# Kernel tuning notes

Measured on AMD Instinct MI355X. Metric: run time of the kernel, lower is better.

Reference implementation:

```python
import jax, jax.numpy as jnp
import numpy as np

B, T, C, H, HD = 2, 2048, 2048, 16, 128
RD = HD // 2          # rope_dim = 64 (32 complex pairs)
KVR, QR = 512, 1024   # kv_lora_rank, q_lora_rank


def setup_inputs() -> dict:
    key = jax.random.key(0)
    ks = jax.random.split(key, 10)
    s = 0.02
    x = jax.random.normal(ks[0], (B, T, C), jnp.float32)
    w_dq  = jax.random.normal(ks[1], (C, QR),     jnp.float32) * s
    w_uq  = jax.random.normal(ks[2], (QR, H * HD), jnp.float32) * s
    w_dkv = jax.random.normal(ks[3], (C, KVR),    jnp.float32) * s
    w_uk  = jax.random.normal(ks[4], (KVR, H * HD), jnp.float32) * s
    w_uv  = jax.random.normal(ks[5], (KVR, H * HD), jnp.float32) * s
    w_qr  = jax.random.normal(ks[6], (QR, H * RD), jnp.float32) * s
    w_kr  = jax.random.normal(ks[7], (C, H * RD), jnp.float32) * s
    w_o   = jax.random.normal(ks[8], (H * HD, C), jnp.float32) * s
    # rotary frequencies for the rope_dim part (rope_dim//2 = 32 complex freqs)
    inv_freq = 1.0 / (10000.0 ** (jnp.arange(0, RD, 2, dtype=jnp.float32) / RD))
    ang = jnp.arange(T, dtype=jnp.float32)[:, None] * inv_freq[None, :]  # (T, 32)
    return {"x": x, "w_dq": w_dq, "w_uq": w_uq, "w_dkv": w_dkv, "w_uk": w_uk,
            "w_uv": w_uv, "w_qr": w_qr, "w_kr": w_kr, "w_o": w_o,
            "freqs_cos": jnp.cos(ang), "freqs_sin": jnp.sin(ang)}


def _apply_rope(t, cos, sin):
    # t: (B, T, H, rd); cos/sin: (T, rd//2). Complex rotation on adjacent pairs.
    tr, ti = t[..., 0::2], t[..., 1::2]
    c = cos[None, :, None, :]
    s = sin[None, :, None, :]
    out_r = tr * c - ti * s
    out_i = tr * s + ti * c
    return jnp.stack([out_r, out_i], axis=-1).reshape(t.shape)


def reference(x, w_dq, w_uq, w_dkv, w_uk, w_uv, w_qr, w_kr, w_o, freqs_cos, freqs_sin):
    b, t, _ = x.shape
    # low-rank KV path
    c_kv = x @ w_dkv                                   # (B,T,KVR)
    k_c = (c_kv @ w_uk).reshape(b, t, H, HD)
    v   = (c_kv @ w_uv).reshape(b, t, H, HD)
    # low-rank Q path
    c_q = x @ w_dq                                     # (B,T,QR)
    q_c = (c_q @ w_uq).reshape(b, t, H, HD)
    # decoupled rope parts
    q_r = (c_q @ w_qr).reshape(b, t, H, RD)
    k_r = (x @ w_kr).reshape(b, t, H, RD)
    q_r = _apply_rope(q_r, freqs_cos, freqs_sin)
    k_r = _apply_rope(k_r, freqs_cos, freqs_sin)
    # concat content + rope -> head dim D = HD + RD
    q = jnp.concatenate([q_c, q_r], axis=-1).transpose(0, 2, 1, 3)  # (B,H,T,D)
    k = jnp.concatenate([k_c, k_r], axis=-1).transpose(0, 2, 1, 3)
    v = v.transpose(0, 2, 1, 3)                                     # (B,H,T,HD)
    d = q.shape[-1]
    scores = jnp.einsum('bhqd,bhkd->bhqk', q, k) / jnp.sqrt(jnp.float32(d))
    causal = jnp.tril(jnp.ones((t, t), dtype=bool))
    scores = jnp.where(causal[None, None], scores, jnp.float32(-1e30))
    att = jax.nn.softmax(scores, axis=-1)
    out = jnp.einsum('bhqk,bhkd->bhqd', att, v)        # (B,H,T,HD)
    out = out.transpose(0, 2, 1, 3).reshape(b, t, H * HD)
    return out @ w_o
```

## Files before the change

kernel.cpp:

```cpp
#include <hip/hip_runtime.h>

typedef unsigned short ushort_t;
typedef __attribute__((ext_vector_type(8))) short bs8;
typedef __attribute__((ext_vector_type(4))) float f32x4;
typedef __attribute__((ext_vector_type(4))) unsigned short u16x4;

#define DEV __device__ __forceinline__

DEV unsigned short f2bf(float f){
  unsigned u = __float_as_uint(f);
  u += 0x7fffu + ((u >> 16) & 1u);
  return (unsigned short)(u >> 16);
}
DEV float bf2f(unsigned short h){ return __uint_as_float(((unsigned)h) << 16); }

DEV unsigned cvt_pk_bf16(float lo, float hi){
  unsigned r;
  asm volatile("v_cvt_pk_bf16_f32 %0, %1, %2" : "=v"(r) : "v"(lo), "v"(hi));
  return r;
}

DEV void gl2lds16(const void* g, void* l){
  __builtin_amdgcn_global_load_lds((const __attribute__((address_space(1))) void*)g,
                                   (__attribute__((address_space(3))) void*)l, 16, 0, 0);
}

DEV void st_out(ushort_t* C, size_t i, float v){ C[i] = f2bf(v); }
DEV void st_out(float*    C, size_t i, float v){ C[i] = v; }

__global__ __launch_bounds__(256) void cast_x(const float* __restrict__ in,
                                              ushort_t* __restrict__ outb){
  size_t i = ((size_t)blockIdx.x * 256 + threadIdx.x) * 4;
  float4 v = *(const float4*)(in + i);
  u16x4 o;
  o[0] = f2bf(v.x); o[1] = f2bf(v.y); o[2] = f2bf(v.z); o[3] = f2bf(v.w);
  *(u16x4*)(outb + i) = o;
}

__global__ __launch_bounds__(256) void tcast_all(
    const float* __restrict__ s0, const float* __restrict__ s1,
    const float* __restrict__ s2, const float* __restrict__ s3,
    const float* __restrict__ s4, const float* __restrict__ s5,
    const float* __restrict__ s6, const float* __restrict__ s7,
    ushort_t* __restrict__ d0, ushort_t* __restrict__ d1,
    ushort_t* __restrict__ d2, ushort_t* __restrict__ d3,
    ushort_t* __restrict__ d4, ushort_t* __restrict__ d5,
    ushort_t* __restrict__ d6, ushort_t* __restrict__ d7){
  __shared__ float tile[32][33];
  const int bid = blockIdx.x;
  const float* src; ushort_t* dst; int K, N, loc;
  if      (bid <  2048){ src=s0; dst=d0; K=2048; N=1024; loc=bid; }
  else if (bid <  3072){ src=s1; dst=d1; K=2048; N=512;  loc=bid-2048; }
  else if (bid <  5120){ src=s2; dst=d2; K=2048; N=1024; loc=bid-3072; }
  else if (bid <  7168){ src=s3; dst=d3; K=1024; N=2048; loc=bid-5120; }
  else if (bid <  8192){ src=s4; dst=d4; K=1024; N=1024; loc=bid-7168; }
  else if (bid <  9216){ src=s5; dst=d5; K=512;  N=2048; loc=bid-8192; }
  else if (bid < 10240){ src=s6; dst=d6; K=512;  N=2048; loc=bid-9216; }
  else                 { src=s7; dst=d7; K=2048; N=2048; loc=bid-10240; }
  const int nx = N >> 5;
  const int n0 = (loc % nx) << 5, k0 = (loc / nx) << 5;
  const int tx = threadIdx.x & 31, ty = threadIdx.x >> 5;
  for (int r = ty; r < 32; r += 8)
    tile[r][tx] = src[(size_t)(k0 + r) * N + n0 + tx];
  __syncthreads();
  for (int r = ty; r < 32; r += 8)
    dst[(size_t)(n0 + r) * K + k0 + tx] = f2bf(tile[tx][r]);
}

__global__ __launch_bounds__(256) void transpose_v(const ushort_t* __restrict__ v, int ldv,
                                                   ushort_t* __restrict__ vT){
  __shared__ ushort_t tile[32][33];
  int bh = blockIdx.z; int b = bh >> 4, h = bh & 15;
  int t0 = blockIdx.x * 32, d0 = blockIdx.y * 32;
  int tx = threadIdx.x, ty = threadIdx.y;
  for (int r = ty; r < 32; r += 8)
    tile[r][tx] = v[((size_t)(b * 2048 + t0 + r)) * ldv + h * 128 + d0 + tx];
  __syncthreads();
  for (int r = ty; r < 32; r += 8)
    vT[((size_t)bh * 128 + d0 + r) * 2048 + t0 + tx] = tile[tx][r];
}

DEV void gemm_core(const ushort_t* __restrict__ A, int lda,
                   const ushort_t* __restrict__ BT, int K,
                   int m0, int n0, ushort_t* lds, f32x4 (&acc)[8][4]){
  const int tid = threadIdx.x, lane = tid & 63, wid = tid >> 6;
  const int l15 = lane & 15, lhi = lane >> 4;
  const int wr = wid >> 2, wc = wid & 3;

  const int trow = tid >> 3;
  const int tcsrc = (tid & 7) ^ (trow & 7);
  const ushort_t* gA[2][2];
  const ushort_t* gB[2][2];
#pragma unroll
  for (int h = 0; h < 2; ++h)
#pragma unroll
    for (int i = 0; i < 2; ++i){
      gA[h][i] = A  + (size_t)(m0 + h * 128 + i * 64 + trow) * lda + tcsrc * 8;
      gB[h][i] = BT + (size_t)(n0 + h * 128 + i * 64 + trow) * K   + tcsrc * 8;
    }

  auto STAGE_A = [&](int buf, int h, int kt){
    gl2lds16(gA[h][0] + (size_t)kt * 64, lds + buf * 32768 + h * 8192 + tid * 8);
    gl2lds16(gA[h][1] + (size_t)kt * 64, lds + buf * 32768 + h * 8192 + 4096 + tid * 8);
  };
  auto STAGE_B = [&](int buf, int h, int kt){
    gl2lds16(gB[h][0] + (size_t)kt * 64, lds + buf * 32768 + 16384 + h * 8192 + tid * 8);
    gl2lds16(gB[h][1] + (size_t)kt * 64, lds + buf * 32768 + 16384 + h * 8192 + 4096 + tid * 8);
  };

  const int ck0 = ((lhi) ^ (l15 & 7)) << 3;
  const int ck1 = ((4 + lhi) ^ (l15 & 7)) << 3;

  bs8 aF[4][2], bLo[2][2], bHi[2][2];

  auto RDA = [&](int buf, int mq){
#pragma unroll
    for (int m = 0; m < 4; ++m){
      const ushort_t* r = lds + buf * 32768 + wr * 8192 + ((mq + m) * 16 + l15) * 64;
      aF[m][0] = *(const bs8*)(r + ck0);
      aF[m][1] = *(const bs8*)(r + ck1);
    }
  };
  auto RDB = [&](int buf, int nq, bs8 (&br)[2][2]){
#pragma unroll
    for (int n = 0; n < 2; ++n){
      const ushort_t* r = lds + buf * 32768 + 16384 + (wc >> 1) * 8192 +
                          ((wc & 1) * 64 + (nq + n) * 16 + l15) * 64;
      br[n][0] = *(const bs8*)(r + ck0);
      br[n][1] = *(const bs8*)(r + ck1);
    }
  };
  auto MMA = [&](int mq, int nq, bs8 (&br)[2][2]){
    __builtin_amdgcn_s_setprio(1);
#pragma unroll
    for (int m = 0; m < 4; ++m)
#pragma unroll
      for (int n = 0; n < 2; ++n){
        acc[mq + m][nq + n] = __builtin_amdgcn_mfma_f32_16x16x32_bf16(aF[m][0], br[n][0], acc[mq + m][nq + n], 0, 0, 0);
        acc[mq + m][nq + n] = __builtin_amdgcn_mfma_f32_16x16x32_bf16(aF[m][1], br[n][1], acc[mq + m][nq + n], 0, 0, 0);
      }
    __builtin_amdgcn_s_setprio(0);
  };

#define BAR() __builtin_amdgcn_s_barrier()
#define LGK() asm volatile("s_waitcnt lgkmcnt(0)" ::: "memory")
#define VMC4() asm volatile("s_waitcnt vmcnt(4)" ::: "memory")

  const int nkt = K >> 6;
  const int nIter = K >> 7;

  STAGE_A(0, 0, 0); STAGE_A(0, 1, 0); STAGE_B(0, 0, 0); STAGE_B(0, 1, 0);
  STAGE_B(1, 0, 1); STAGE_B(1, 1, 1);
  VMC4();
  BAR();

  for (int it = 0; it < nIter; ++it){
    const int kt1 = 2 * it + 1;
    int kt2 = 2 * it + 2; if (kt2 > nkt - 1) kt2 = nkt - 1;
    int kt3 = 2 * it + 3; if (kt3 > nkt - 1) kt3 = nkt - 1;
    RDA(0, 0); RDB(0, 0, bLo);
    STAGE_A(1, 0, kt1);
    BAR(); LGK(); MMA(0, 0, bLo); BAR();
    RDB(0, 2, bHi);
    STAGE_A(1, 1, kt1);
    BAR(); LGK(); MMA(0, 2, bHi); BAR();
    RDA(0, 4);
    STAGE_B(0, 0, kt2);
    BAR(); LGK(); MMA(4, 0, bLo); BAR();
    STAGE_B(0, 1, kt2);
    BAR(); LGK(); MMA(4, 2, bHi);
    VMC4(); BAR();
    RDA(1, 0); RDB(1, 0, bLo);
    STAGE_A(0, 0, kt2);
    BAR(); LGK(); MMA(0, 0, bLo); BAR();
    RDB(1, 2, bHi);
    STAGE_A(0, 1, kt2);
    BAR(); LGK(); MMA(0, 2, bHi); BAR();
    RDA(1, 4);
    STAGE_B(1, 0, kt3);
    BAR(); LGK(); MMA(4, 0, bLo); BAR();
    STAGE_B(1, 1, kt3);
    BAR(); LGK(); MMA(4, 2, bHi);
    VMC4(); BAR();
  }
#undef BAR
#undef LGK
#undef VMC4
}

template<int EPI, typename OT>
DEV void gemm_epi(f32x4 (&acc)[8][4], OT* __restrict__ C, int N, int m0, int n0,
                  ushort_t* __restrict__ aux,
                  const float* __restrict__ fcp, const float* __restrict__ fsp){
  const int tid = threadIdx.x, lane = tid & 63, wid = tid >> 6;
  const int l15 = lane & 15, lhi = lane >> 4;
  const int wr = wid >> 2, wc = wid & 3;
  const float SC = (EPI == 2) ? (0.07216878364870323f * 1.4426950408889634f) : 1.0f;
  const int RBASE = (EPI == 1) ? 1536 : 2048;
#pragma unroll
  for (int m = 0; m < 8; ++m){
    const int r = m0 + wr * 128 + m * 16 + lhi * 4;
#pragma unroll
    for (int n = 0; n < 4; ++n){
      const int c = n0 + wc * 64 + n * 16 + l15;
      if (EPI == 0){
#pragma unroll
        for (int j = 0; j < 4; ++j)
          st_out(C, (size_t)(r + j) * N + c, acc[m][n][j]);
      } else if ((EPI == 1 && c < 1536)){
#pragma unroll
        for (int j = 0; j < 4; ++j)
          C[(size_t)(r + j) * 1536 + c] = (OT)f2bf(acc[m][n][j]);
      } else if (EPI == 2 && c < 2048){
        int hh = c >> 7, d = c & 127;
#pragma unroll
        for (int j = 0; j < 4; ++j){
          int rr = r + j, bb = rr >> 11, tt = rr & 2047;
          aux[((size_t)(bb * 16 + hh) * 2048 + tt) * 192 + d] = f2bf(acc[m][n][j] * SC);
        }
      } else if (EPI == 3 && c < 2048){
        int hh = c >> 7, d = c & 127;
#pragma unroll
        for (int j = 0; j < 4; ++j){
          int rr = r + j, bb = rr >> 11, tt = rr & 2047;
          aux[((size_t)(bb * 16 + hh) * 2048 + tt) * 192 + d] = f2bf(acc[m][n][j]);
        }
      } else if (EPI == 3){
#pragma unroll
        for (int j = 0; j < 4; ++j)
          C[(size_t)(r + j) * 2048 + (c - 2048)] = (OT)f2bf(acc[m][n][j]);
      } else {
        int cr = c - RBASE;
        int hh = cr >> 6, dr = cr & 63, ii = dr >> 1;
#pragma unroll
        for (int j = 0; j < 4; ++j){
          int rr = r + j, bb = rr >> 11, tt = rr & 2047;
          float v = acc[m][n][j] * SC;
          float pv = __shfl_xor(v, 1);
          float co = fcp[tt * 32 + ii], si = fsp[tt * 32 + ii];
          float o = (l15 & 1) ? fmaf(pv, si, v * co) : fmaf(-pv, si, v * co);
          aux[((size_t)(bb * 16 + hh) * 2048 + tt) * 192 + 128 + dr] = f2bf(o);
        }
      }
    }
  }
}

template<int EPI, typename OT>
__global__ __launch_bounds__(512, 2) void gemm256(const ushort_t* __restrict__ A, int lda,
                                                  const ushort_t* __restrict__ BT,
                                                  OT* __restrict__ C,
                                                  int M, int N, int K,
                                                  ushort_t* __restrict__ aux,
                                                  const float* __restrict__ fcp,
                                                  const float* __restrict__ fsp){
  __shared__ __align__(16) ushort_t lds[65536];
  const int nbx = M >> 8;
  const int nwg = gridDim.x;
  const int orig = blockIdx.x;
  const int wg = (orig & 7) * (nwg >> 3) + (orig >> 3);
  const int m0 = (wg % nbx) << 8;
  const int n0 = (wg / nbx) << 8;
  f32x4 acc[8][4] = {};
  gemm_core(A, lda, BT, K, m0, n0, lds, acc);
  gemm_epi<EPI, OT>(acc, C, N, m0, n0, aux, fcp, fsp);
}

__global__ __launch_bounds__(512, 2) void gemm23(const ushort_t* __restrict__ A2,
                                                 const ushort_t* __restrict__ BT2,
                                                 const ushort_t* __restrict__ A3,
                                                 const ushort_t* __restrict__ BT3,
                                                 ushort_t* __restrict__ vb,
                                                 ushort_t* __restrict__ Qa,
                                                 ushort_t* __restrict__ Ka,
                                                 const float* __restrict__ fcp,
                                                 const float* __restrict__ fsp){
  __shared__ __align__(16) ushort_t lds[65536];
  const int nwg = gridDim.x;
  const int orig = blockIdx.x;
  const int wg = (orig & 7) * (nwg >> 3) + (orig >> 3);
  f32x4 acc[8][4] = {};
  if (wg < 192){
    const int m0 = (wg % 16) << 8, n0 = (wg / 16) << 8;
    gemm_core(A2, 1536, BT2, 1024, m0, n0, lds, acc);
    gemm_epi<2, ushort_t>(acc, nullptr, 3072, m0, n0, Qa, fcp, fsp);
  } else {
    const int g = wg - 192;
    const int m0 = (g % 16) << 8, n0 = (g / 16) << 8;
    gemm_core(A3, 1536, BT3, 512, m0, n0, lds, acc);
    gemm_epi<3, ushort_t>(acc, vb, 4096, m0, n0, Ka, fcp, fsp);
  }
}

__global__ __launch_bounds__(512, 1) void gemm4_128(const ushort_t* __restrict__ A, int lda,
                                                    const ushort_t* __restrict__ BT,
                                                    float* __restrict__ C,
                                                    int M, int N, int K){
  __shared__ __align__(16) ushort_t lds[49152];
  const int tid = threadIdx.x, lane = tid & 63, wid = tid >> 6;
  const int l15 = lane & 15, lhi = lane >> 4;
  const int wr = wid >> 1, wc = wid & 1;

  const int nbx = M >> 8;
  const int nwg = gridDim.x;
  const int orig = blockIdx.x;
  const int wg = (orig & 7) * (nwg >> 3) + (orig >> 3);
  const int m0 = (wg % nbx) << 8;
  const int n0 = (wg / nbx) << 7;

  const int trow = tid >> 3;
  const int tcsrc = (tid & 7) ^ (trow & 7);
  const ushort_t* gA[2][2];
  const ushort_t* gB[2];
#pragma unroll
  for (int h = 0; h < 2; ++h)
#pragma unroll
    for (int i = 0; i < 2; ++i)
      gA[h][i] = A + (size_t)(m0 + h * 128 + i * 64 + trow) * lda + tcsrc * 8;
#pragma unroll
  for (int i = 0; i < 2; ++i)
    gB[i] = BT + (size_t)(n0 + i * 64 + trow) * K + tcsrc * 8;

  auto STAGE_A = [&](int buf, int h, int kt){
    gl2lds16(gA[h][0] + (size_t)kt * 64, lds + buf * 24576 + h * 8192 + tid * 8);
    gl2lds16(gA[h][1] + (size_t)kt * 64, lds + buf * 24576 + h * 8192 + 4096 + tid * 8);
  };
  auto STAGE_B = [&](int buf, int kt){
    gl2lds16(gB[0] + (size_t)kt * 64, lds + buf * 24576 + 16384 + tid * 8);
    gl2lds16(gB[1] + (size_t)kt * 64, lds + buf * 24576 + 16384 + 4096 + tid * 8);
  };

  const int ck0 = ((lhi) ^ (l15 & 7)) << 3;
  const int ck1 = ((4 + lhi) ^ (l15 & 7)) << 3;

  f32x4 acc[4][4] = {};
  bs8 aF[2][2], bLo[2][2], bHi[2][2];

  auto RDA = [&](int buf, int mq){
#pragma unroll
    for (int m = 0; m < 2; ++m){
      const int rowin = (wr & 1) * 64 + (mq + m) * 16 + l15;
      const ushort_t* r = lds + buf * 24576 + (wr >> 1) * 8192 + rowin * 64;
      aF[m][0] = *(const bs8*)(r + ck0);
      aF[m][1] = *(const bs8*)(r + ck1);
    }
  };
  auto RDB = [&](int buf, int nq, bs8 (&br)[2][2]){
#pragma unroll
    for (int n = 0; n < 2; ++n){
      const int row = wc * 64 + (nq + n) * 16 + l15;
      const ushort_t* r = lds + buf * 24576 + 16384 + row * 64;
      br[n][0] = *(const bs8*)(r + ck0);
      br[n][1] = *(const bs8*)(r + ck1);
    }
  };
  auto MMA = [&](int mq, int nq, bs8 (&br)[2][2]){
    __builtin_amdgcn_s_setprio(1);
#pragma unroll
    for (int m = 0; m < 2; ++m)
#pragma unroll
      for (int n = 0; n < 2; ++n){
        acc[mq + m][nq + n] = __builtin_amdgcn_mfma_f32_16x16x32_bf16(aF[m][0], br[n][0], acc[mq + m][nq + n], 0, 0, 0);
        acc[mq + m][nq + n] = __builtin_amdgcn_mfma_f32_16x16x32_bf16(aF[m][1], br[n][1], acc[mq + m][nq + n], 0, 0, 0);
      }
    __builtin_amdgcn_s_setprio(0);
  };

#define BAR() __builtin_amdgcn_s_barrier()
#define LGK() asm volatile("s_waitcnt lgkmcnt(0)" ::: "memory")
#define VMC2() asm volatile("s_waitcnt vmcnt(2)" ::: "memory")

  const int nkt = K >> 6;
  const int nIter = K >> 7;

  STAGE_A(0, 0, 0); STAGE_A(0, 1, 0); STAGE_B(0, 0);
  STAGE_B(1, 1);
  VMC2();
  BAR();

  for (int it = 0; it < nIter; ++it){
    const int kt1 = 2 * it + 1;
    int kt2 = 2 * it + 2; if (kt2 > nkt - 1) kt2 = nkt - 1;
    int kt3 = 2 * it + 3; if (kt3 > nkt - 1) kt3 = nkt - 1;
    RDA(0, 0); RDB(0, 0, bLo);
    STAGE_A(1, 0, kt1);
    BAR(); LGK(); MMA(0, 0, bLo); BAR();
    RDB(0, 2, bHi);
    STAGE_A(1, 1, kt1);
    BAR(); LGK(); MMA(0, 2, bHi); BAR();
    RDA(0, 2);
    STAGE_B(0, kt2);
    BAR(); LGK(); MMA(2, 0, bLo); BAR();
    BAR(); LGK(); MMA(2, 2, bHi);
    VMC2(); BAR();
    RDA(1, 0); RDB(1, 0, bLo);
    STAGE_A(0, 0, kt2);
    BAR(); LGK(); MMA(0, 0, bLo); BAR();
    RDB(1, 2, bHi);
    STAGE_A(0, 1, kt2);
    BAR(); LGK(); MMA(0, 2, bHi); BAR();
    RDA(1, 2);
    STAGE_B(1, kt3);
    BAR(); LGK(); MMA(2, 0, bLo); BAR();
    BAR(); LGK(); MMA(2, 2, bHi);
    VMC2(); BAR();
  }
#undef BAR
#undef LGK
#undef VMC2

#pragma unroll
  for (int m = 0; m < 4; ++m){
    const int r = m0 + wr * 64 + m * 16 + lhi * 4;
#pragma unroll
    for (int n = 0; n < 4; ++n){
      const int c = n0 + wc * 64 + n * 16 + l15;
#pragma unroll
      for (int j = 0; j < 4; ++j)
        C[(size_t)(r + j) * N + c] = acc[m][n][j];
    }
  }
}

__global__ __launch_bounds__(512, 1) void attn_kernel(const ushort_t* __restrict__ Qa,
                                                      const ushort_t* __restrict__ Ka,
                                                      const ushort_t* __restrict__ VT,
                                                      ushort_t* __restrict__ O){
  __shared__ __align__(16) ushort_t lds[40960];
  const int tid = threadIdx.x, lane = tid & 63, wid = tid >> 6;
  const int bh = blockIdx.x, p = blockIdx.y;
  const int b = bh >> 4, h = bh & 15;
  const int qb0 = 15 - p, qb1 = p;
  const int nkt0 = 2 * qb0 + 2;
  const int NT = 34;
  const int l15 = lane & 15, lhi = lane >> 4;

  const ushort_t* Kbh = Ka + (size_t)bh * 2048 * 192;
  const ushort_t* Vbh = VT + (size_t)bh * 128 * 2048;

  const ushort_t* ksrc[3];
#pragma unroll
  for (int i = 0; i < 3; ++i){
    int c = i * 512 + tid;
    int row = c / 24, col = c % 24;
    int hk = (row & 3) | (((row >> 3) & 1) << 2);
    ksrc[i] = Kbh + (size_t)row * 192 + (col ^ hk) * 8;
  }
  const ushort_t* vsrc[2];
#pragma unroll
  for (int i = 0; i < 2; ++i){
    int c = i * 512 + tid;
    int d = c >> 3, col = c & 7;
    vsrc[i] = Vbh + (size_t)d * 2048 + (col ^ (d & 7)) * 8;
  }

  auto STAGE = [&](int ft, int buf){
    int kt = (ft < nkt0) ? ft : ft - nkt0;
#pragma unroll
    for (int i = 0; i < 3; ++i)
      gl2lds16(ksrc[i] + (size_t)kt * 12288, lds + buf * 12288 + (i * 512 + tid) * 8);
#pragma unroll
    for (int i = 0; i < 2; ++i)
      gl2lds16(vsrc[i] + kt * 64, lds + 24576 + buf * 8192 + (i * 512 + tid) * 8);
  };

  bs8 qf[6];
  auto LOADQ = [&](int qb){
    const size_t qrow = ((size_t)bh * 2048 + qb * 128 + wid * 16 + l15) * 192;
#pragma unroll
    for (int kc = 0; kc < 6; ++kc)
      qf[kc] = *(const bs8*)(Qa + qrow + kc * 32 + lhi * 8);
  };

  f32x4 acc[8] = {};
  float mrow = -1e30f, lrow = 0.f;

  auto EPI = [&](int qb){
    float rl = 1.0f / lrow;
    int t = qb * 128 + wid * 16 + l15;
#pragma unroll
    for (int f = 0; f < 8; ++f){
      u16x4 o;
#pragma unroll
      for (int j = 0; j < 4; ++j) o[j] = f2bf(acc[f][j] * rl);
      *(u16x4*)(O + ((size_t)b * 2048 + t) * 2048 + h * 128 + f * 16 + lhi * 4) = o;
    }
  };

  const int hkr = (l15 & 3) | (((l15 >> 2) & 1) << 2);

#define BARR() __builtin_amdgcn_s_barrier()
#define LGK0() asm volatile("s_waitcnt lgkmcnt(0)" ::: "memory")
#define VMC(n) asm volatile("s_waitcnt vmcnt(" #n ")" ::: "memory")

  LOADQ(qb0);
  STAGE(0, 0);
  STAGE(1, 1);
  VMC(5);
  BARR();

  for (int ft = 0; ft < NT; ++ft){
    if (ft == nkt0){
      EPI(qb0);
#pragma unroll
      for (int f = 0; f < 8; ++f) acc[f] = (f32x4){0.f, 0.f, 0.f, 0.f};
      mrow = -1e30f; lrow = 0.f;
      LOADQ(qb1);
    }
    const int seg = (ft >= nkt0) ? 1 : 0;
    const int kt = seg ? ft - nkt0 : ft;
    const int qb = seg ? qb1 : qb0;
    const int qm0 = qb << 7;
    const int mylast = 2 * qb + (wid >> 2);
    const int cur = ft & 1;
    const ushort_t* Kb = lds + cur * 12288;
    const ushort_t* Vb = lds + 24576 + cur * 8192;

    if (kt <= mylast){
      f32x4 s[4] = {};
      __builtin_amdgcn_s_setprio(1);
#pragma unroll
      for (int kc = 0; kc < 6; ++kc){
        bs8 kf4[4];
#pragma unroll
        for (int m = 0; m < 4; ++m){
          int row = ((m >> 1) << 5) + ((l15 >> 2) << 3) + ((m & 1) << 2) + (l15 & 3);
          kf4[m] = *(const bs8*)(Kb + row * 192 + (((kc * 4 + lhi) ^ hkr) << 3));
        }
#pragma unroll
        for (int m = 0; m < 4; ++m)
          s[m] = __builtin_amdgcn_mfma_f32_16x16x32_bf16(kf4[m], qf[kc], s[m], 0, 0, 0);
      }
      __builtin_amdgcn_s_setprio(0);

      const bool noMask = (kt * 64 + 63) <= (qm0 + wid * 16);
      const int qi = qm0 + wid * 16 + l15;
      float rmax = -3e38f;
#pragma unroll
      for (int m = 0; m < 4; ++m)
#pragma unroll
        for (int j = 0; j < 4; ++j){
          float sv = s[m][j];
          if (!noMask){
            int ki = kt * 64 + ((m >> 1) << 5) + (lhi << 3) + ((m & 1) << 2) + j;
            if (ki > qi) sv = -3e38f;
          }
          s[m][j] = sv;
          rmax = fmaxf(rmax, sv);
        }
      rmax = fmaxf(rmax, __shfl_xor(rmax, 16));
      rmax = fmaxf(rmax, __shfl_xor(rmax, 32));
      if (!__all(rmax <= mrow + 8.f)){
        float mnew = fmaxf(mrow, rmax);
        float osc = exp2f(mrow - mnew);
        lrow *= osc;
#pragma unroll
        for (int f = 0; f < 8; ++f) acc[f] *= osc;
        mrow = mnew;
      }
      float rsum = 0.f;
#pragma unroll
      for (int m = 0; m < 4; ++m)
#pragma unroll
        for (int j = 0; j < 4; ++j){
          float pv = exp2f(s[m][j] - mrow);
          s[m][j] = pv;
          rsum += pv;
        }
      rsum += __shfl_xor(rsum, 16);
      rsum += __shfl_xor(rsum, 32);
      lrow += rsum;

      bs8 pb[2];
#pragma unroll
      for (int kc2 = 0; kc2 < 2; ++kc2){
        union { bs8 v; unsigned u[4]; } pu;
#pragma unroll
        for (int half = 0; half < 2; ++half){
          const f32x4& sv = s[2 * kc2 + half];
          pu.u[2 * half]     = cvt_pk_bf16(sv[0], sv[1]);
          pu.u[2 * half + 1] = cvt_pk_bf16(sv[2], sv[3]);
        }
        pb[kc2] = pu.v;
      }

      __builtin_amdgcn_s_setprio(1);
#pragma unroll
      for (int kc2 = 0; kc2 < 2; ++kc2)
#pragma unroll
        for (int f = 0; f < 8; ++f){
          bs8 vf = *(const bs8*)(Vb + (f * 16 + l15) * 64 + (((kc2 * 4 + lhi) ^ (l15 & 7)) << 3));
          acc[f] = __builtin_amdgcn_mfma_f32_16x16x32_bf16(vf, pb[kc2], acc[f], 0, 0, 0);
        }
      __builtin_amdgcn_s_setprio(0);
    }

    LGK0();
    BARR();
    if (ft + 2 < NT){
      STAGE(ft + 2, cur);
      VMC(5);
    } else {
      VMC(0);
    }
    BARR();
  }
#undef BARR
#undef LGK0
#undef VMC

  EPI(qb1);
}

extern "C" void kernel_launch(void* const* d_in, const int* in_sizes, int n_in,
                              void* d_out, int out_size, void* d_ws, size_t ws_size,
                              hipStream_t stream){
  constexpr int Bc = 2, Tc = 2048, Cc = 2048, Hc = 16, HDc = 128, RDc = 64, KVRc = 512, QRc = 1024;
  constexpr int Mx = Bc * Tc;
  const float* x     = (const float*)d_in[0];
  const float* w_dq  = (const float*)d_in[1];
  const float* w_uq  = (const float*)d_in[2];
  const float* w_dkv = (const float*)d_in[3];
  const float* w_uk  = (const float*)d_in[4];
  const float* w_uv  = (const float*)d_in[5];
  const float* w_qr  = (const float*)d_in[6];
  const float* w_kr  = (const float*)d_in[7];
  const float* w_o   = (const float*)d_in[8];
  const float* fc    = (const float*)d_in[9];
  const float* fs    = (const float*)d_in[10];
  float* out = (float*)d_out;

  char* ws = (char*)d_ws;
  size_t off = 0;
  auto alloc = [&](size_t elems) -> ushort_t* {
    ushort_t* p = (ushort_t*)(ws + off);
    off += ((elems * 2) + 255) & ~(size_t)255;
    return p;
  };
  ushort_t* xb    = alloc((size_t)Mx * Cc);
  ushort_t* wdqT  = alloc((size_t)QRc * Cc);
  ushort_t* wdkvT = alloc((size_t)KVRc * Cc);
  ushort_t* wkrT  = alloc((size_t)(Hc * RDc) * Cc);
  ushort_t* wuqT  = alloc((size_t)(Hc * HDc) * QRc);
  ushort_t* wqrT  = alloc((size_t)(Hc * RDc) * QRc);
  ushort_t* wukT  = alloc((size_t)(Hc * HDc) * KVRc);
  ushort_t* wuvT  = alloc((size_t)(Hc * HDc) * KVRc);
  ushort_t* woT   = alloc((size_t)Cc * (Hc * HDc));
  ushort_t* comb1 = alloc((size_t)Mx * 1536);
  ushort_t* vb    = alloc((size_t)Mx * 2048);
  ushort_t* Qa    = alloc((size_t)Bc * Hc * Tc * 192);
  ushort_t* Ka    = alloc((size_t)Bc * Hc * Tc * 192);
  ushort_t* vT    = alloc((size_t)Bc * Hc * HDc * Tc);
  ushort_t* O     = xb;

  cast_x<<<dim3(((size_t)Mx * Cc) / 1024), 256, 0, stream>>>(x, xb);

  tcast_all<<<dim3(14336), 256, 0, stream>>>(w_dq, w_dkv, w_kr, w_uq, w_qr, w_uk, w_uv, w_o,
                                             wdqT, wdkvT, wkrT, wuqT, wqrT, wukT, wuvT, woT);

  gemm256<1, ushort_t><<<dim3((Mx / 256) * (2560 / 256)), 512, 0, stream>>>(
      xb, Cc, wdqT, comb1, Mx, 2560, Cc, Ka, fc, fs);
  gemm23<<<dim3(448), 512, 0, stream>>>(comb1, wuqT, comb1 + QRc, wukT, vb, Qa, Ka, fc, fs);

  transpose_v<<<dim3(Tc / 32, HDc / 32, Bc * Hc), dim3(32, 8), 0, stream>>>(vb, 2048, vT);

  attn_kernel<<<dim3(Bc * Hc, 8), 512, 0, stream>>>(Qa, Ka, vT, O);

  gemm4_128<<<dim3(256), 512, 0, stream>>>(O, Hc * HDc, woT, out, Mx, Cc, Hc * HDc);
}
```

Measured before the change: 306.5 us.

## Fuse V transpose into GEMM epilogue and split attention into per-query-block workgroups

The V up-projection epilogue now writes V directly in the transposed per-head layout, which removes the separate transpose_v kernel and the intermediate V buffer. The attention kernel no longer pairs a long and a short query block in one workgroup for causal load balance. It launches one workgroup per 128-row query block (16 per head), with the launch-bounds occupancy hint relaxed. This gives more parallelism and simpler control flow, but the workload per workgroup becomes unbalanced. The transposed epilogue stores 4 consecutive t values per lane, so its global writes may be less coalesced.

```diff
diff --git a/kernel.cpp b/kernel.cpp
--- a/kernel.cpp
+++ b/kernel.cpp
@@ -67,19 +67,6 @@
     dst[(size_t)(n0 + r) * K + k0 + tx] = f2bf(tile[tx][r]);
 }
 
-__global__ __launch_bounds__(256) void transpose_v(const ushort_t* __restrict__ v, int ldv,
-                                                   ushort_t* __restrict__ vT){
-  __shared__ ushort_t tile[32][33];
-  int bh = blockIdx.z; int b = bh >> 4, h = bh & 15;
-  int t0 = blockIdx.x * 32, d0 = blockIdx.y * 32;
-  int tx = threadIdx.x, ty = threadIdx.y;
-  for (int r = ty; r < 32; r += 8)
-    tile[r][tx] = v[((size_t)(b * 2048 + t0 + r)) * ldv + h * 128 + d0 + tx];
-  __syncthreads();
-  for (int r = ty; r < 32; r += 8)
-    vT[((size_t)bh * 128 + d0 + r) * 2048 + t0 + tx] = tile[tx][r];
-}
-
 DEV void gemm_core(const ushort_t* __restrict__ A, int lda,
                    const ushort_t* __restrict__ BT, int K,
                    int m0, int n0, ushort_t* lds, f32x4 (&acc)[8][4]){
@@ -226,9 +213,13 @@
           aux[((size_t)(bb * 16 + hh) * 2048 + tt) * 192 + d] = f2bf(acc[m][n][j]);
         }
       } else if (EPI == 3){
-#pragma unroll
-        for (int j = 0; j < 4; ++j)
-          C[(size_t)(r + j) * 2048 + (c - 2048)] = (OT)f2bf(acc[m][n][j]);
+        int cv = c - 2048;
+        int hh = cv >> 7, d = cv & 127;
+        int bb = r >> 11, tt = r & 2047;
+        u16x4 o;
+#pragma unroll
+        for (int j = 0; j < 4; ++j) o[j] = f2bf(acc[m][n][j]);
+        *(u16x4*)((ushort_t*)C + ((size_t)(bb * 16 + hh) * 128 + d) * 2048 + tt) = o;
       } else {
         int cr = c - RBASE;
         int hh = cr >> 6, dr = cr & 63, ii = dr >> 1;
@@ -270,7 +261,7 @@
                                                  const ushort_t* __restrict__ BT2,
                                                  const ushort_t* __restrict__ A3,
                                                  const ushort_t* __restrict__ BT3,
-                                                 ushort_t* __restrict__ vb,
+                                                 ushort_t* __restrict__ vT,
                                                  ushort_t* __restrict__ Qa,
                                                  ushort_t* __restrict__ Ka,
                                                  const float* __restrict__ fcp,
@@ -288,7 +279,7 @@
     const int g = wg - 192;
     const int m0 = (g % 16) << 8, n0 = (g / 16) << 8;
     gemm_core(A3, 1536, BT3, 512, m0, n0, lds, acc);
-    gemm_epi<3, ushort_t>(acc, vb, 4096, m0, n0, Ka, fcp, fsp);
+    gemm_epi<3, ushort_t>(acc, vT, 4096, m0, n0, Ka, fcp, fsp);
   }
 }
 
@@ -422,17 +413,17 @@
   }
 }
 
-__global__ __launch_bounds__(512, 1) void attn_kernel(const ushort_t* __restrict__ Qa,
-                                                      const ushort_t* __restrict__ Ka,
-                                                      const ushort_t* __restrict__ VT,
-                                                      ushort_t* __restrict__ O){
+__global__ __launch_bounds__(512) void attn_kernel(const ushort_t* __restrict__ Qa,
+                                                   const ushort_t* __restrict__ Ka,
+                                                   const ushort_t* __restrict__ VT,
+                                                   ushort_t* __restrict__ O){
   __shared__ __align__(16) ushort_t lds[40960];
   const int tid = threadIdx.x, lane = tid & 63, wid = tid >> 6;
-  const int bh = blockIdx.x, p = blockIdx.y;
+  const int bh = blockIdx.x;
+  const int qb = 15 - blockIdx.y;
   const int b = bh >> 4, h = bh & 15;
-  const int qb0 = 15 - p, qb1 = p;
-  const int nkt0 = 2 * qb0 + 2;
-  const int NT = 34;
+  const int qm0 = qb << 7;
+  const int nkt = 2 * qb + 2;
   const int l15 = lane & 15, lhi = lane >> 4;
 
   const ushort_t* Kbh = Ka + (size_t)bh * 2048 * 192;
@@ -454,8 +445,7 @@
     vsrc[i] = Vbh + (size_t)d * 2048 + (col ^ (d & 7)) * 8;
   }
 
-  auto STAGE = [&](int ft, int buf){
-    int kt = (ft < nkt0) ? ft : ft - nkt0;
+  auto STAGE = [&](int kt, int buf){
 #pragma unroll
     for (int i = 0; i < 3; ++i)
       gl2lds16(ksrc[i] + (size_t)kt * 12288, lds + buf * 12288 + (i * 512 + tid) * 8);
@@ -465,54 +455,30 @@
   };
 
   bs8 qf[6];
-  auto LOADQ = [&](int qb){
-    const size_t qrow = ((size_t)bh * 2048 + qb * 128 + wid * 16 + l15) * 192;
+  {
+    const size_t qrow = ((size_t)bh * 2048 + qm0 + wid * 16 + l15) * 192;
 #pragma unroll
     for (int kc = 0; kc < 6; ++kc)
       qf[kc] = *(const bs8*)(Qa + qrow + kc * 32 + lhi * 8);
-  };
+  }
 
   f32x4 acc[8] = {};
   float mrow = -1e30f, lrow = 0.f;
 
-  auto EPI = [&](int qb){
-    float rl = 1.0f / lrow;
-    int t = qb * 128 + wid * 16 + l15;
-#pragma unroll
-    for (int f = 0; f < 8; ++f){
-      u16x4 o;
-#pragma unroll
-      for (int j = 0; j < 4; ++j) o[j] = f2bf(acc[f][j] * rl);
-      *(u16x4*)(O + ((size_t)b * 2048 + t) * 2048 + h * 128 + f * 16 + lhi * 4) = o;
-    }
-  };
-
+  const int mylast = 2 * qb + (wid >> 2);
   const int hkr = (l15 & 3) | (((l15 >> 2) & 1) << 2);
 
 #define BARR() __builtin_amdgcn_s_barrier()
 #define LGK0() asm volatile("s_waitcnt lgkmcnt(0)" ::: "memory")
 #define VMC(n) asm volatile("s_waitcnt vmcnt(" #n ")" ::: "memory")
 
-  LOADQ(qb0);
   STAGE(0, 0);
   STAGE(1, 1);
   VMC(5);
   BARR();
 
-  for (int ft = 0; ft < NT; ++ft){
-    if (ft == nkt0){
-      EPI(qb0);
-#pragma unroll
-      for (int f = 0; f < 8; ++f) acc[f] = (f32x4){0.f, 0.f, 0.f, 0.f};
-      mrow = -1e30f; lrow = 0.f;
-      LOADQ(qb1);
-    }
-    const int seg = (ft >= nkt0) ? 1 : 0;
-    const int kt = seg ? ft - nkt0 : ft;
-    const int qb = seg ? qb1 : qb0;
-    const int qm0 = qb << 7;
-    const int mylast = 2 * qb + (wid >> 2);
-    const int cur = ft & 1;
+  for (int kt = 0; kt < nkt; ++kt){
+    const int cur = kt & 1;
     const ushort_t* Kb = lds + cur * 12288;
     const ushort_t* Vb = lds + 24576 + cur * 8192;
 
@@ -597,8 +563,8 @@
 
     LGK0();
     BARR();
-    if (ft + 2 < NT){
-      STAGE(ft + 2, cur);
+    if (kt + 2 < nkt){
+      STAGE(kt + 2, cur);
       VMC(5);
     } else {
       VMC(0);
@@ -609,7 +575,17 @@
 #undef LGK0
 #undef VMC
 
-  EPI(qb1);
+  {
+    float rl = 1.0f / lrow;
+    int t = qm0 + wid * 16 + l15;
+#pragma unroll
+    for (int f = 0; f < 8; ++f){
+      u16x4 o;
+#pragma unroll
+      for (int j = 0; j < 4; ++j) o[j] = f2bf(acc[f][j] * rl);
+      *(u16x4*)(O + ((size_t)b * 2048 + t) * 2048 + h * 128 + f * 16 + lhi * 4) = o;
+    }
+  }
 }
 
 extern "C" void kernel_launch(void* const* d_in, const int* in_sizes, int n_in,
@@ -647,7 +623,6 @@
   ushort_t* wuvT  = alloc((size_t)(Hc * HDc) * KVRc);
   ushort_t* woT   = alloc((size_t)Cc * (Hc * HDc));
   ushort_t* comb1 = alloc((size_t)Mx * 1536);
-  ushort_t* vb    = alloc((size_t)Mx * 2048);
   ushort_t* Qa    = alloc((size_t)Bc * Hc * Tc * 192);
   ushort_t* Ka    = alloc((size_t)Bc * Hc * Tc * 192);
   ushort_t* vT    = alloc((size_t)Bc * Hc * HDc * Tc);
@@ -660,11 +635,9 @@
 
   gemm256<1, ushort_t><<<dim3((Mx / 256) * (2560 / 256)), 512, 0, stream>>>(
       xb, Cc, wdqT, comb1, Mx, 2560, Cc, Ka, fc, fs);
-  gemm23<<<dim3(448), 512, 0, stream>>>(comb1, wuqT, comb1 + QRc, wukT, vb, Qa, Ka, fc, fs);
-
-  transpose_v<<<dim3(Tc / 32, HDc / 32, Bc * Hc), dim3(32, 8), 0, stream>>>(vb, 2048, vT);
-
-  attn_kernel<<<dim3(Bc * Hc, 8), 512, 0, stream>>>(Qa, Ka, vT, O);
+  gemm23<<<dim3(448), 512, 0, stream>>>(comb1, wuqT, comb1 + QRc, wukT, vT, Qa, Ka, fc, fs);
+
+  attn_kernel<<<dim3(Bc * Hc, 16), 512, 0, stream>>>(Qa, Ka, vT, O);
 
   gemm4_128<<<dim3(256), 512, 0, stream>>>(O, Hc * HDc, woT, out, Mx, Cc, Hc * HDc);
 }
```

Measured after the change: 285.4 us. -6.9%, faster.
